# Performance work log

Measured on AMD Instinct MI355X. Metric: run time of the kernel, lower is better.

The kernel has to match this reference:

```python
import math
import jax, jax.numpy as jnp
import numpy as np

B, S, D, H = 2, 4096, 512, 8
DH = D // H


def setup_inputs() -> dict:
    key = jax.random.key(0)
    ks = jax.random.split(key, 12)
    lim = 1.0 / math.sqrt(D)
    u = lambda k, shp: jax.random.uniform(k, shp, jnp.float32, -lim, lim)
    return {
        "x": jax.random.normal(ks[0], (B, S, D), jnp.float32),
        "gamma": jax.random.uniform(ks[1], (B, S, 1), jnp.float32),
        "Wq": u(ks[2], (D, D)), "bq": u(ks[3], (D,)),
        "Wk": u(ks[4], (D, D)), "bk": u(ks[5], (D,)),
        "Wv": u(ks[6], (D, D)), "bv": u(ks[7], (D,)),
        "Wo": u(ks[8], (D, D)), "bo": u(ks[9], (D,)),
    }


def reference(x, gamma, Wq, bq, Wk, bk, Wv, bv, Wo, bo):
    b, s, d = x.shape
    # projections (torch Linear: x @ W.T + b), split heads -> [B,H,S,DH]
    def proj(W, bias):
        return (x @ W.T + bias).reshape(b, s, H, DH).transpose(0, 2, 1, 3)
    q, k, v = proj(Wq, bq), proj(Wk, bk), proj(Wv, bv)

    scores = jnp.einsum("bhsd,bhtd->bhst", q, k) / math.sqrt(DH)  # [B,H,S,S]
    causal = jnp.triu(jnp.ones((s, s), bool), k=1)  # True above diagonal
    neg_inf = jnp.float32(-jnp.inf)
    scores = jnp.where(causal[None, None], neg_inf, scores)

    # hyperbolic positional bias: -log1p(gamma_i * max(i-j, 0) + 1e-8)
    pos = jnp.arange(s)
    delta = jnp.clip(pos[:, None] - pos[None, :], 0).astype(jnp.float32)  # [S,S]
    gamma_q = gamma[:, :, 0][:, :, None]  # [B,S,1]
    hyper = -jnp.log1p(gamma_q * delta + 1e-8)  # [B,S,S]
    hyper = jnp.where(causal[None], neg_inf, hyper)
    scores = scores + hyper[:, None]  # [B,H,S,S]

    attn = jax.nn.softmax(scores, axis=-1)
    out = jnp.einsum("bhst,bhtd->bhsd", attn, v)  # [B,H,S,DH]
    out = out.transpose(0, 2, 1, 3).reshape(b, s, d)
    return out @ Wo.T + bo
```

## Files before the change

### kernel.cpp

```cpp
#include <hip/hip_runtime.h>
#include <hip/hip_bf16.h>

#define Bb 2
#define Ss 4096
#define Dd 512
#define Hh 8
#define DHh 64

typedef __attribute__((ext_vector_type(8))) short short8;
typedef __attribute__((ext_vector_type(4))) float floatx4;

static __device__ __forceinline__ ushort bfbits(float f) {
  union { __hip_bfloat16 h; ushort u; } cv;
  cv.h = __float2bfloat16(f);
  return cv.u;
}

__global__ void cvt_all(const float* __restrict__ x,
                        const float* __restrict__ w0, const float* __restrict__ w1,
                        const float* __restrict__ w2, const float* __restrict__ w3,
                        ushort* __restrict__ out) {
  const int XN4 = (Bb * Ss * Dd) / 4;
  const int WN4 = (Dd * Dd) / 4;
  int i = blockIdx.x * blockDim.x + threadIdx.x;
  if (i >= XN4 + 4 * WN4) return;
  const float* s; int li;
  if (i < XN4) { s = x; li = i; }
  else {
    int t = i - XN4; int j = t >> 16; li = t & (WN4 - 1);
    s = (j == 0) ? w0 : (j == 1) ? w1 : (j == 2) ? w2 : w3;
  }
  float4 f = ((const float4*)s)[li];
  ushort4 u;
  u.x = bfbits(f.x); u.y = bfbits(f.y); u.z = bfbits(f.z); u.w = bfbits(f.w);
  ((ushort4*)out)[i] = u;
}

static __device__ __forceinline__ int vperm(int s0) {
  int kb = (s0 >> 4) & 3, gq = (s0 >> 2) & 3;
  return (s0 & ~63) | ((kb >> 1) << 5) | (gq << 3) | ((kb & 1) << 2);
}

#define LD32(buf, k0)                                                          \
  af[buf][0] = *(const short8*)(ap + (k0));                                    \
  af[buf][1] = *(const short8*)(ap + 16 * 512 + (k0));                         \
  _Pragma("unroll")                                                            \
  for (int ns = 0; ns < 4; ++ns)                                               \
    bfr[buf][ns] = *(const short8*)(bp + (size_t)ns * 16 * 512 + (k0));

__global__ __launch_bounds__(256) void qkv_gemm(
    const ushort* __restrict__ xb,
    const ushort* __restrict__ Wq, const ushort* __restrict__ Wk, const ushort* __restrict__ Wv,
    const float* __restrict__ bq, const float* __restrict__ bk, const float* __restrict__ bv,
    ushort* __restrict__ qo, ushort* __restrict__ ko, ushort* __restrict__ vo)
{
  int mb = blockIdx.x / 24, nbt = blockIdx.x % 24;
  int which = nbt >> 3, nb = nbt & 7;
  const ushort* Bw  = (which == 0) ? Wq : (which == 1) ? Wk : Wv;
  const float* bias = (which == 0) ? bq : (which == 1) ? bk : bv;
  int lane = threadIdx.x & 63, w = threadIdx.x >> 6;
  int g = lane >> 4, ln = lane & 15;
  int m0 = mb * 128 + w * 32;
  const ushort* ap = xb + (size_t)(m0 + ln) * 512 + g * 8;
  const ushort* bp = Bw + (size_t)(nb * 64 + ln) * 512 + g * 8;
  floatx4 acc[2][4] = {};
  short8 af[2][2], bfr[2][4];
  LD32(0, 0)
#pragma unroll
  for (int it = 0; it < 16; ++it) {
    int cur = it & 1;
    if (it < 15) { LD32(cur ^ 1, (it + 1) * 32) }
#pragma unroll
    for (int ns = 0; ns < 4; ++ns) {
      acc[0][ns] = __builtin_amdgcn_mfma_f32_16x16x32_bf16(af[cur][0], bfr[cur][ns], acc[0][ns], 0, 0, 0);
      acc[1][ns] = __builtin_amdgcn_mfma_f32_16x16x32_bf16(af[cur][1], bfr[cur][ns], acc[1][ns], 0, 0, 0);
    }
  }
  float scale = (which == 0) ? 0.125f : 1.0f;
#pragma unroll
  for (int rb = 0; rb < 2; ++rb)
#pragma unroll
    for (int ns = 0; ns < 4; ++ns) {
      int col = nb * 64 + ns * 16 + ln;
      float bv_ = bias[col];
      int hh = col >> 6, dh = col & 63;
      if (which == 2) {
        int i0 = m0 + rb * 16 + g * 4;
        int bI = i0 >> 12, s0 = i0 & (Ss - 1);
        ushort4 pk;
        pk.x = bfbits(acc[rb][ns][0] + bv_);
        pk.y = bfbits(acc[rb][ns][1] + bv_);
        pk.z = bfbits(acc[rb][ns][2] + bv_);
        pk.w = bfbits(acc[rb][ns][3] + bv_);
        *(ushort4*)(vo + (((size_t)bI * Hh + hh) * DHh + dh) * Ss + vperm(s0)) = pk;
      } else {
        ushort* outp = (which == 0) ? qo : ko;
#pragma unroll
        for (int r = 0; r < 4; ++r) {
          int i = m0 + rb * 16 + g * 4 + r;
          int bI = i >> 12, s = i & (Ss - 1);
          outp[(((size_t)bI * Hh + hh) * Ss + s) * DHh + dh] = bfbits((acc[rb][ns][r] + bv_) * scale);
        }
      }
    }
}

__global__ __launch_bounds__(256) void gemm_out(
    const ushort* __restrict__ A, const ushort* __restrict__ Bw,
    const float* __restrict__ bias, float* __restrict__ outp)
{
  int mb = blockIdx.x >> 3, nb = blockIdx.x & 7;
  int lane = threadIdx.x & 63, w = threadIdx.x >> 6;
  int g = lane >> 4, ln = lane & 15;
  int m0 = mb * 128 + w * 32;
  const ushort* ap = A + (size_t)(m0 + ln) * 512 + g * 8;
  const ushort* bp = Bw + (size_t)(nb * 64 + ln) * 512 + g * 8;
  floatx4 acc[2][4] = {};
  short8 af[2][2], bfr[2][4];
  LD32(0, 0)
#pragma unroll
  for (int it = 0; it < 16; ++it) {
    int cur = it & 1;
    if (it < 15) { LD32(cur ^ 1, (it + 1) * 32) }
#pragma unroll
    for (int ns = 0; ns < 4; ++ns) {
      acc[0][ns] = __builtin_amdgcn_mfma_f32_16x16x32_bf16(af[cur][0], bfr[cur][ns], acc[0][ns], 0, 0, 0);
      acc[1][ns] = __builtin_amdgcn_mfma_f32_16x16x32_bf16(af[cur][1], bfr[cur][ns], acc[1][ns], 0, 0, 0);
    }
  }
#pragma unroll
  for (int rb = 0; rb < 2; ++rb)
#pragma unroll
    for (int ns = 0; ns < 4; ++ns) {
      int col = nb * 64 + ns * 16 + ln;
      float bv_ = bias[col];
#pragma unroll
      for (int r = 0; r < 4; ++r)
        outp[(size_t)(m0 + rb * 16 + g * 4 + r) * 512 + col] = acc[rb][ns][r] + bv_;
    }
}

__global__ __launch_bounds__(256, 2) void flash5(
    const ushort* __restrict__ q, const ushort* __restrict__ k,
    const ushort* __restrict__ vt, const float* __restrict__ gamma,
    ushort* __restrict__ o)
{
  __shared__ __align__(16) float Pmrg[2][64][34];
  __shared__ __align__(16) ushort Tb[2][16 * 72];

  int z = blockIdx.x;
  int j = (z ^ (z >> 8)) & 3;
  int bh = (z >> 2) & 15;
  int w16 = z >> 6;
  int u = (j == 0) ? w16 : (j == 1) ? 31 - w16 : (j == 2) ? 32 + w16 : 63 - w16;
  int b = bh >> 3, hh = bh & 7;
  int tid = threadIdx.x;
  int wv = tid >> 6, lane = tid & 63;
  int qsel = wv >> 1, half = wv & 1;
  int g = lane >> 4, ln = lane & 15;
  int t = 2 * u + qsel;
  int q0 = t * 32;
  int ktm = u;
  int nkt = u + 1;
  int h = (nkt + 1) >> 1;
  int lo = half ? h : 0, hi = half ? nkt : h;

  const ushort* qp = q + ((size_t)bh * Ss + q0 + ln) * DHh + g * 8;
  short8 qf00 = *(const short8*)qp;
  short8 qf01 = *(const short8*)(qp + 32);
  short8 qf10 = *(const short8*)(qp + 16 * DHh);
  short8 qf11 = *(const short8*)(qp + 16 * DHh + 32);

  const ushort* kp = k + ((size_t)bh * Ss + ln) * DHh + g * 8;
  const ushort* vp = vt + ((size_t)bh * DHh + ln) * Ss + g * 8;

  int qrow0 = q0 + ln, qrow1 = q0 + 16 + ln;
  float gm0 = gamma[(size_t)b * Ss + qrow0];
  float gm1 = gamma[(size_t)b * Ss + qrow1];
  float l2[2] = {0.0f, 0.0f};
  floatx4 oacc[2][4] = {};

  short8 kfl[4], kfh[4], vf[8];
  int kb0 = lo * 64;
#pragma unroll
  for (int ns = 0; ns < 4; ++ns) {
    kfl[ns] = *(const short8*)(kp + (size_t)(kb0 + ns * 16) * DHh);
    kfh[ns] = *(const short8*)(kp + (size_t)(kb0 + ns * 16) * DHh + 32);
  }
#pragma unroll
  for (int cc = 0; cc < 8; ++cc)
    vf[cc] = *(const short8*)(vp + (size_t)((cc & 3) * 16) * Ss + kb0 + (cc >> 2) * 32);

  for (int kt = lo; kt < hi; ++kt) {
    int kbase = kt * 64;
    float sv[2][16];
#pragma unroll
    for (int ns = 0; ns < 4; ++ns) {
      floatx4 z0 = {}, z1 = {};
      z0 = __builtin_amdgcn_mfma_f32_16x16x32_bf16(kfl[ns], qf00, z0, 0, 0, 0);
      z0 = __builtin_amdgcn_mfma_f32_16x16x32_bf16(kfh[ns], qf01, z0, 0, 0, 0);
      z1 = __builtin_amdgcn_mfma_f32_16x16x32_bf16(kfl[ns], qf10, z1, 0, 0, 0);
      z1 = __builtin_amdgcn_mfma_f32_16x16x32_bf16(kfh[ns], qf11, z1, 0, 0, 0);
#pragma unroll
      for (int r = 0; r < 4; ++r) { sv[0][ns * 4 + r] = z0[r]; sv[1][ns * 4 + r] = z1[r]; }
    }
    if (kt + 1 < hi) {
      const ushort* kn = kp + (size_t)(kbase + 64) * DHh;
#pragma unroll
      for (int ns = 0; ns < 4; ++ns) {
        kfl[ns] = *(const short8*)(kn + (size_t)(ns * 16) * DHh);
        kfh[ns] = *(const short8*)(kn + (size_t)(ns * 16) * DHh + 32);
      }
    }
    bool last = (kt == ktm);
    short8 pfrag[2][2];
#pragma unroll
    for (int qb = 0; qb < 2; ++qb) {
      int qrow = qb ? qrow1 : qrow0;
      float gm = qb ? gm1 : gm0;
      int db = qrow - kbase - g * 4;
      if (last) {
#pragma unroll
        for (int e = 0; e < 16; ++e)
          if (db - (e >> 2) * 16 - (e & 3) < 0) sv[qb][e] = -1e30f;
      }
      float rs = 0.0f;
#pragma unroll
      for (int e = 0; e < 16; ++e) {
        float delta = fmaxf((float)(db - (e >> 2) * 16 - (e & 3)), 0.0f);
        float wt = __builtin_amdgcn_rcpf(fmaf(gm, delta, 1.0f));
        float pv = __expf(sv[qb][e]) * wt;
        rs += pv;
        sv[qb][e] = pv;
      }
      l2[qb] += rs;
#pragma unroll
      for (int c = 0; c < 2; ++c) {
        short8 pk;
#pragma unroll
        for (int jj = 0; jj < 4; ++jj) {
          ((ushort*)&pk)[jj]     = bfbits(sv[qb][(2 * c) * 4 + jj]);
          ((ushort*)&pk)[jj + 4] = bfbits(sv[qb][(2 * c + 1) * 4 + jj]);
        }
        pfrag[qb][c] = pk;
      }
    }
#pragma unroll
    for (int c = 0; c < 2; ++c)
#pragma unroll
      for (int ds = 0; ds < 4; ++ds) {
        oacc[0][ds] = __builtin_amdgcn_mfma_f32_16x16x32_bf16(vf[c * 4 + ds], pfrag[0][c], oacc[0][ds], 0, 0, 0);
        oacc[1][ds] = __builtin_amdgcn_mfma_f32_16x16x32_bf16(vf[c * 4 + ds], pfrag[1][c], oacc[1][ds], 0, 0, 0);
      }
    if (kt + 1 < hi) {
#pragma unroll
      for (int cc = 0; cc < 8; ++cc)
        vf[cc] = *(const short8*)(vp + (size_t)((cc & 3) * 16) * Ss + kbase + 64 + (cc >> 2) * 32);
    }
  }

  if (half) {
#pragma unroll
    for (int qb = 0; qb < 2; ++qb)
#pragma unroll
      for (int ds = 0; ds < 4; ++ds)
#pragma unroll
        for (int r = 0; r < 4; ++r)
          Pmrg[qsel][lane][qb * 16 + ds * 4 + r] = oacc[qb][ds][r];
    Pmrg[qsel][lane][32] = l2[0];
    Pmrg[qsel][lane][33] = l2[1];
  }
  __syncthreads();
  if (!half) {
#pragma unroll
    for (int qb = 0; qb < 2; ++qb) {
#pragma unroll
      for (int ds = 0; ds < 4; ++ds)
#pragma unroll
        for (int r = 0; r < 4; ++r)
          oacc[qb][ds][r] += Pmrg[qsel][lane][qb * 16 + ds * 4 + r];
      float l = l2[qb] + Pmrg[qsel][lane][32 + qb];
      l += __shfl_xor(l, 16);
      l += __shfl_xor(l, 32);
      float linv = 1.0f / l;
      ushort* tb = &Tb[qsel][0];
#pragma unroll
      for (int ds = 0; ds < 4; ++ds)
#pragma unroll
        for (int r = 0; r < 4; ++r)
          tb[ln * 72 + ds * 16 + g * 4 + r] = bfbits(oacc[qb][ds][r] * linv);
      short8 v0 = *(const short8*)(tb + ln * 72 + g * 16);
      short8 v1 = *(const short8*)(tb + ln * 72 + g * 16 + 8);
      size_t oa = ((size_t)b * Ss + q0 + qb * 16 + ln) * Dd + hh * DHh + g * 16;
      *(short8*)(o + oa) = v0;
      *(short8*)(o + oa + 8) = v1;
    }
  }
}

extern "C" void kernel_launch(void* const* d_in, const int* in_sizes, int n_in,
                              void* d_out, int out_size, void* d_ws, size_t ws_size,
                              hipStream_t stream) {
  const float* x     = (const float*)d_in[0];
  const float* gamma = (const float*)d_in[1];
  const float* Wq    = (const float*)d_in[2];
  const float* bq    = (const float*)d_in[3];
  const float* Wk    = (const float*)d_in[4];
  const float* bk    = (const float*)d_in[5];
  const float* Wv    = (const float*)d_in[6];
  const float* bv    = (const float*)d_in[7];
  const float* Wo    = (const float*)d_in[8];
  const float* bo    = (const float*)d_in[9];

  const size_t NX = (size_t)Bb * Ss * Dd;
  const size_t NW = (size_t)Dd * Dd;
  ushort* xb  = (ushort*)d_ws;
  ushort* Wqb = xb + NX;
  ushort* Wkb = Wqb + NW;
  ushort* Wvb = Wkb + NW;
  ushort* Wob = Wvb + NW;
  ushort* qb  = Wob + NW;
  ushort* kb  = qb + NX;
  ushort* vtb = kb + NX;
  ushort* ab  = vtb + NX;

  const int total4 = (int)(NX / 4 + 4 * (NW / 4));
  cvt_all<<<(total4 + 255) / 256, 256, 0, stream>>>(x, Wq, Wk, Wv, Wo, xb);

  qkv_gemm<<<64 * 24, 256, 0, stream>>>(xb, Wqb, Wkb, Wvb, bq, bk, bv, qb, kb, vtb);

  flash5<<<1024, 256, 0, stream>>>(qb, kb, vtb, gamma, ab);

  gemm_out<<<512, 256, 0, stream>>>(ab, Wob, bo, (float*)d_out);
}
```

Before: 310.5 us.

## Enlarge QKV GEMM tiles, pair causal tiles per block, truncate bf16 packing

The QKV projection GEMM now gives each wave a 64x64 output tile (4x4 MFMA fragments), so each block covers 128x128 and half as many blocks launch, raising operand reuse per load. The flash attention kernel processes two complementary causal query tiles (u and 63-u) in one persistent block, which evens out work per block and halves the grid. It also changes how the key-tile split between the two halves is chosen in the second pass. P-fragment packing now truncates fp32 to bf16 by taking the high bits instead of rounding, which saves ALU work but adds a small precision bias.

```diff
diff --git a/kernel.cpp b/kernel.cpp
--- a/kernel.cpp
+++ b/kernel.cpp
@@ -14,6 +14,11 @@
   union { __hip_bfloat16 h; ushort u; } cv;
   cv.h = __float2bfloat16(f);
   return cv.u;
+}
+
+static __device__ __forceinline__ unsigned int packhi(float a, float b) {
+  union { float f; unsigned int u; } ca, cb; ca.f = a; cb.f = b;
+  return (ca.u >> 16) | (cb.u & 0xffff0000u);
 }
 
 __global__ void cvt_all(const float* __restrict__ x,
@@ -41,69 +46,79 @@
   return (s0 & ~63) | ((kb >> 1) << 5) | (gq << 3) | ((kb & 1) << 2);
 }
 
+#define LDQK(buf, k0)                                                          \
+  _Pragma("unroll")                                                            \
+  for (int rb = 0; rb < 4; ++rb)                                               \
+    af[buf][rb] = *(const short8*)(ap + (size_t)rb * 16 * 512 + (k0));         \
+  _Pragma("unroll")                                                            \
+  for (int cb = 0; cb < 4; ++cb)                                               \
+    bf[buf][cb] = *(const short8*)(bp + (size_t)cb * 16 * 512 + (k0));
+
+__global__ __launch_bounds__(256) void qkv_gemm(
+    const ushort* __restrict__ xb,
+    const ushort* __restrict__ Wq, const ushort* __restrict__ Wk, const ushort* __restrict__ Wv,
+    const float* __restrict__ bq, const float* __restrict__ bk, const float* __restrict__ bv,
+    ushort* __restrict__ qo, ushort* __restrict__ ko, ushort* __restrict__ vo)
+{
+  int mb = blockIdx.x / 12, rest = blockIdx.x % 12;
+  int which = rest >> 2, nb = rest & 3;
+  const ushort* Bw  = (which == 0) ? Wq : (which == 1) ? Wk : Wv;
+  const float* bias = (which == 0) ? bq : (which == 1) ? bk : bv;
+  int lane = threadIdx.x & 63, w = threadIdx.x >> 6;
+  int wr = w & 1, wc = w >> 1;
+  int g = lane >> 4, ln = lane & 15;
+  int m0 = mb * 128 + wr * 64;
+  int c0 = nb * 128 + wc * 64;
+  const ushort* ap = xb + (size_t)(m0 + ln) * 512 + g * 8;
+  const ushort* bp = Bw + (size_t)(c0 + ln) * 512 + g * 8;
+  floatx4 acc[4][4] = {};
+  short8 af[2][4], bf[2][4];
+  LDQK(0, 0)
+#pragma unroll
+  for (int it = 0; it < 16; ++it) {
+    int cur = it & 1;
+    if (it < 15) { LDQK(cur ^ 1, (it + 1) * 32) }
+#pragma unroll
+    for (int rb = 0; rb < 4; ++rb)
+#pragma unroll
+      for (int cb = 0; cb < 4; ++cb)
+        acc[rb][cb] = __builtin_amdgcn_mfma_f32_16x16x32_bf16(af[cur][rb], bf[cur][cb], acc[rb][cb], 0, 0, 0);
+  }
+  float scale = (which == 0) ? 0.125f : 1.0f;
+#pragma unroll
+  for (int rb = 0; rb < 4; ++rb)
+#pragma unroll
+    for (int cb = 0; cb < 4; ++cb) {
+      int col = c0 + cb * 16 + ln;
+      float bv_ = bias[col];
+      int hh = col >> 6, dh = col & 63;
+      if (which == 2) {
+        int i0 = m0 + rb * 16 + g * 4;
+        int bI = i0 >> 12, s0 = i0 & (Ss - 1);
+        ushort4 pk;
+        pk.x = bfbits(acc[rb][cb][0] + bv_);
+        pk.y = bfbits(acc[rb][cb][1] + bv_);
+        pk.z = bfbits(acc[rb][cb][2] + bv_);
+        pk.w = bfbits(acc[rb][cb][3] + bv_);
+        *(ushort4*)(vo + (((size_t)bI * Hh + hh) * DHh + dh) * Ss + vperm(s0)) = pk;
+      } else {
+        ushort* outp = (which == 0) ? qo : ko;
+#pragma unroll
+        for (int r = 0; r < 4; ++r) {
+          int i = m0 + rb * 16 + g * 4 + r;
+          int bI = i >> 12, s = i & (Ss - 1);
+          outp[(((size_t)bI * Hh + hh) * Ss + s) * DHh + dh] = bfbits((acc[rb][cb][r] + bv_) * scale);
+        }
+      }
+    }
+}
+
 #define LD32(buf, k0)                                                          \
   af[buf][0] = *(const short8*)(ap + (k0));                                    \
   af[buf][1] = *(const short8*)(ap + 16 * 512 + (k0));                         \
   _Pragma("unroll")                                                            \
   for (int ns = 0; ns < 4; ++ns)                                               \
     bfr[buf][ns] = *(const short8*)(bp + (size_t)ns * 16 * 512 + (k0));
-
-__global__ __launch_bounds__(256) void qkv_gemm(
-    const ushort* __restrict__ xb,
-    const ushort* __restrict__ Wq, const ushort* __restrict__ Wk, const ushort* __restrict__ Wv,
-    const float* __restrict__ bq, const float* __restrict__ bk, const float* __restrict__ bv,
-    ushort* __restrict__ qo, ushort* __restrict__ ko, ushort* __restrict__ vo)
-{
-  int mb = blockIdx.x / 24, nbt = blockIdx.x % 24;
-  int which = nbt >> 3, nb = nbt & 7;
-  const ushort* Bw  = (which == 0) ? Wq : (which == 1) ? Wk : Wv;
-  const float* bias = (which == 0) ? bq : (which == 1) ? bk : bv;
-  int lane = threadIdx.x & 63, w = threadIdx.x >> 6;
-  int g = lane >> 4, ln = lane & 15;
-  int m0 = mb * 128 + w * 32;
-  const ushort* ap = xb + (size_t)(m0 + ln) * 512 + g * 8;
-  const ushort* bp = Bw + (size_t)(nb * 64 + ln) * 512 + g * 8;
-  floatx4 acc[2][4] = {};
-  short8 af[2][2], bfr[2][4];
-  LD32(0, 0)
-#pragma unroll
-  for (int it = 0; it < 16; ++it) {
-    int cur = it & 1;
-    if (it < 15) { LD32(cur ^ 1, (it + 1) * 32) }
-#pragma unroll
-    for (int ns = 0; ns < 4; ++ns) {
-      acc[0][ns] = __builtin_amdgcn_mfma_f32_16x16x32_bf16(af[cur][0], bfr[cur][ns], acc[0][ns], 0, 0, 0);
-      acc[1][ns] = __builtin_amdgcn_mfma_f32_16x16x32_bf16(af[cur][1], bfr[cur][ns], acc[1][ns], 0, 0, 0);
-    }
-  }
-  float scale = (which == 0) ? 0.125f : 1.0f;
-#pragma unroll
-  for (int rb = 0; rb < 2; ++rb)
-#pragma unroll
-    for (int ns = 0; ns < 4; ++ns) {
-      int col = nb * 64 + ns * 16 + ln;
-      float bv_ = bias[col];
-      int hh = col >> 6, dh = col & 63;
-      if (which == 2) {
-        int i0 = m0 + rb * 16 + g * 4;
-        int bI = i0 >> 12, s0 = i0 & (Ss - 1);
-        ushort4 pk;
-        pk.x = bfbits(acc[rb][ns][0] + bv_);
-        pk.y = bfbits(acc[rb][ns][1] + bv_);
-        pk.z = bfbits(acc[rb][ns][2] + bv_);
-        pk.w = bfbits(acc[rb][ns][3] + bv_);
-        *(ushort4*)(vo + (((size_t)bI * Hh + hh) * DHh + dh) * Ss + vperm(s0)) = pk;
-      } else {
-        ushort* outp = (which == 0) ? qo : ko;
-#pragma unroll
-        for (int r = 0; r < 4; ++r) {
-          int i = m0 + rb * 16 + g * 4 + r;
-          int bI = i >> 12, s = i & (Ss - 1);
-          outp[(((size_t)bI * Hh + hh) * Ss + s) * DHh + dh] = bfbits((acc[rb][ns][r] + bv_) * scale);
-        }
-      }
-    }
-}
 
 __global__ __launch_bounds__(256) void gemm_out(
     const ushort* __restrict__ A, const ushort* __restrict__ Bw,
@@ -140,7 +155,7 @@
     }
 }
 
-__global__ __launch_bounds__(256, 2) void flash5(
+__global__ __launch_bounds__(256, 2) void flash6(
     const ushort* __restrict__ q, const ushort* __restrict__ k,
     const ushort* __restrict__ vt, const float* __restrict__ gamma,
     ushort* __restrict__ o)
@@ -149,151 +164,154 @@
   __shared__ __align__(16) ushort Tb[2][16 * 72];
 
   int z = blockIdx.x;
-  int j = (z ^ (z >> 8)) & 3;
-  int bh = (z >> 2) & 15;
-  int w16 = z >> 6;
-  int u = (j == 0) ? w16 : (j == 1) ? 31 - w16 : (j == 2) ? 32 + w16 : 63 - w16;
+  int bh = z & 15, up = z >> 4;
   int b = bh >> 3, hh = bh & 7;
   int tid = threadIdx.x;
   int wv = tid >> 6, lane = tid & 63;
   int qsel = wv >> 1, half = wv & 1;
   int g = lane >> 4, ln = lane & 15;
-  int t = 2 * u + qsel;
-  int q0 = t * 32;
-  int ktm = u;
-  int nkt = u + 1;
-  int h = (nkt + 1) >> 1;
-  int lo = half ? h : 0, hi = half ? nkt : h;
-
-  const ushort* qp = q + ((size_t)bh * Ss + q0 + ln) * DHh + g * 8;
-  short8 qf00 = *(const short8*)qp;
-  short8 qf01 = *(const short8*)(qp + 32);
-  short8 qf10 = *(const short8*)(qp + 16 * DHh);
-  short8 qf11 = *(const short8*)(qp + 16 * DHh + 32);
 
   const ushort* kp = k + ((size_t)bh * Ss + ln) * DHh + g * 8;
   const ushort* vp = vt + ((size_t)bh * DHh + ln) * Ss + g * 8;
 
-  int qrow0 = q0 + ln, qrow1 = q0 + 16 + ln;
-  float gm0 = gamma[(size_t)b * Ss + qrow0];
-  float gm1 = gamma[(size_t)b * Ss + qrow1];
-  float l2[2] = {0.0f, 0.0f};
-  floatx4 oacc[2][4] = {};
-
-  short8 kfl[4], kfh[4], vf[8];
-  int kb0 = lo * 64;
-#pragma unroll
-  for (int ns = 0; ns < 4; ++ns) {
-    kfl[ns] = *(const short8*)(kp + (size_t)(kb0 + ns * 16) * DHh);
-    kfh[ns] = *(const short8*)(kp + (size_t)(kb0 + ns * 16) * DHh + 32);
-  }
-#pragma unroll
-  for (int cc = 0; cc < 8; ++cc)
-    vf[cc] = *(const short8*)(vp + (size_t)((cc & 3) * 16) * Ss + kb0 + (cc >> 2) * 32);
-
-  for (int kt = lo; kt < hi; ++kt) {
-    int kbase = kt * 64;
-    float sv[2][16];
+#pragma unroll 1
+  for (int rep = 0; rep < 2; ++rep) {
+    int u = rep ? (63 - up) : up;
+    int t = 2 * u + qsel;
+    int q0 = t * 32;
+    int ktm = u;
+    int nkt = u + 1;
+    int h = (nkt + 1 - rep) >> 1;
+    int lo = half ? h : 0, hi = half ? nkt : h;
+
+    const ushort* qp = q + ((size_t)bh * Ss + q0 + ln) * DHh + g * 8;
+    short8 qf00 = *(const short8*)qp;
+    short8 qf01 = *(const short8*)(qp + 32);
+    short8 qf10 = *(const short8*)(qp + 16 * DHh);
+    short8 qf11 = *(const short8*)(qp + 16 * DHh + 32);
+
+    int qrow0 = q0 + ln, qrow1 = q0 + 16 + ln;
+    float gm0 = gamma[(size_t)b * Ss + qrow0];
+    float gm1 = gamma[(size_t)b * Ss + qrow1];
+    float l2[2] = {0.0f, 0.0f};
+    floatx4 oacc[2][4] = {};
+
+    short8 kfl[4], kfh[4], vf[8];
+    int kb0 = lo * 64;
 #pragma unroll
     for (int ns = 0; ns < 4; ++ns) {
-      floatx4 z0 = {}, z1 = {};
-      z0 = __builtin_amdgcn_mfma_f32_16x16x32_bf16(kfl[ns], qf00, z0, 0, 0, 0);
-      z0 = __builtin_amdgcn_mfma_f32_16x16x32_bf16(kfh[ns], qf01, z0, 0, 0, 0);
-      z1 = __builtin_amdgcn_mfma_f32_16x16x32_bf16(kfl[ns], qf10, z1, 0, 0, 0);
-      z1 = __builtin_amdgcn_mfma_f32_16x16x32_bf16(kfh[ns], qf11, z1, 0, 0, 0);
-#pragma unroll
-      for (int r = 0; r < 4; ++r) { sv[0][ns * 4 + r] = z0[r]; sv[1][ns * 4 + r] = z1[r]; }
-    }
-    if (kt + 1 < hi) {
-      const ushort* kn = kp + (size_t)(kbase + 64) * DHh;
+      kfl[ns] = *(const short8*)(kp + (size_t)(kb0 + ns * 16) * DHh);
+      kfh[ns] = *(const short8*)(kp + (size_t)(kb0 + ns * 16) * DHh + 32);
+    }
+#pragma unroll
+    for (int cc = 0; cc < 8; ++cc)
+      vf[cc] = *(const short8*)(vp + (size_t)((cc & 3) * 16) * Ss + kb0 + (cc >> 2) * 32);
+
+    for (int kt = lo; kt < hi; ++kt) {
+      int kbase = kt * 64;
+      float sv[2][16];
 #pragma unroll
       for (int ns = 0; ns < 4; ++ns) {
-        kfl[ns] = *(const short8*)(kn + (size_t)(ns * 16) * DHh);
-        kfh[ns] = *(const short8*)(kn + (size_t)(ns * 16) * DHh + 32);
-      }
-    }
-    bool last = (kt == ktm);
-    short8 pfrag[2][2];
-#pragma unroll
-    for (int qb = 0; qb < 2; ++qb) {
-      int qrow = qb ? qrow1 : qrow0;
-      float gm = qb ? gm1 : gm0;
-      int db = qrow - kbase - g * 4;
-      if (last) {
-#pragma unroll
-        for (int e = 0; e < 16; ++e)
-          if (db - (e >> 2) * 16 - (e & 3) < 0) sv[qb][e] = -1e30f;
-      }
-      float rs = 0.0f;
-#pragma unroll
-      for (int e = 0; e < 16; ++e) {
-        float delta = fmaxf((float)(db - (e >> 2) * 16 - (e & 3)), 0.0f);
-        float wt = __builtin_amdgcn_rcpf(fmaf(gm, delta, 1.0f));
-        float pv = __expf(sv[qb][e]) * wt;
-        rs += pv;
-        sv[qb][e] = pv;
-      }
-      l2[qb] += rs;
-#pragma unroll
-      for (int c = 0; c < 2; ++c) {
-        short8 pk;
-#pragma unroll
-        for (int jj = 0; jj < 4; ++jj) {
-          ((ushort*)&pk)[jj]     = bfbits(sv[qb][(2 * c) * 4 + jj]);
-          ((ushort*)&pk)[jj + 4] = bfbits(sv[qb][(2 * c + 1) * 4 + jj]);
-        }
-        pfrag[qb][c] = pk;
-      }
-    }
-#pragma unroll
-    for (int c = 0; c < 2; ++c)
-#pragma unroll
-      for (int ds = 0; ds < 4; ++ds) {
-        oacc[0][ds] = __builtin_amdgcn_mfma_f32_16x16x32_bf16(vf[c * 4 + ds], pfrag[0][c], oacc[0][ds], 0, 0, 0);
-        oacc[1][ds] = __builtin_amdgcn_mfma_f32_16x16x32_bf16(vf[c * 4 + ds], pfrag[1][c], oacc[1][ds], 0, 0, 0);
-      }
-    if (kt + 1 < hi) {
-#pragma unroll
-      for (int cc = 0; cc < 8; ++cc)
-        vf[cc] = *(const short8*)(vp + (size_t)((cc & 3) * 16) * Ss + kbase + 64 + (cc >> 2) * 32);
-    }
-  }
-
-  if (half) {
-#pragma unroll
-    for (int qb = 0; qb < 2; ++qb)
-#pragma unroll
-      for (int ds = 0; ds < 4; ++ds)
-#pragma unroll
-        for (int r = 0; r < 4; ++r)
-          Pmrg[qsel][lane][qb * 16 + ds * 4 + r] = oacc[qb][ds][r];
-    Pmrg[qsel][lane][32] = l2[0];
-    Pmrg[qsel][lane][33] = l2[1];
-  }
-  __syncthreads();
-  if (!half) {
-#pragma unroll
-    for (int qb = 0; qb < 2; ++qb) {
-#pragma unroll
-      for (int ds = 0; ds < 4; ++ds)
-#pragma unroll
-        for (int r = 0; r < 4; ++r)
-          oacc[qb][ds][r] += Pmrg[qsel][lane][qb * 16 + ds * 4 + r];
-      float l = l2[qb] + Pmrg[qsel][lane][32 + qb];
-      l += __shfl_xor(l, 16);
-      l += __shfl_xor(l, 32);
-      float linv = 1.0f / l;
-      ushort* tb = &Tb[qsel][0];
-#pragma unroll
-      for (int ds = 0; ds < 4; ++ds)
-#pragma unroll
-        for (int r = 0; r < 4; ++r)
-          tb[ln * 72 + ds * 16 + g * 4 + r] = bfbits(oacc[qb][ds][r] * linv);
-      short8 v0 = *(const short8*)(tb + ln * 72 + g * 16);
-      short8 v1 = *(const short8*)(tb + ln * 72 + g * 16 + 8);
-      size_t oa = ((size_t)b * Ss + q0 + qb * 16 + ln) * Dd + hh * DHh + g * 16;
-      *(short8*)(o + oa) = v0;
-      *(short8*)(o + oa + 8) = v1;
+        floatx4 z0 = {}, z1 = {};
+        z0 = __builtin_amdgcn_mfma_f32_16x16x32_bf16(kfl[ns], qf00, z0, 0, 0, 0);
+        z0 = __builtin_amdgcn_mfma_f32_16x16x32_bf16(kfh[ns], qf01, z0, 0, 0, 0);
+        z1 = __builtin_amdgcn_mfma_f32_16x16x32_bf16(kfl[ns], qf10, z1, 0, 0, 0);
+        z1 = __builtin_amdgcn_mfma_f32_16x16x32_bf16(kfh[ns], qf11, z1, 0, 0, 0);
+#pragma unroll
+        for (int r = 0; r < 4; ++r) { sv[0][ns * 4 + r] = z0[r]; sv[1][ns * 4 + r] = z1[r]; }
+      }
+      if (kt + 1 < hi) {
+        const ushort* kn = kp + (size_t)(kbase + 64) * DHh;
+#pragma unroll
+        for (int ns = 0; ns < 4; ++ns) {
+          kfl[ns] = *(const short8*)(kn + (size_t)(ns * 16) * DHh);
+          kfh[ns] = *(const short8*)(kn + (size_t)(ns * 16) * DHh + 32);
+        }
+      }
+      bool last = (kt == ktm);
+      short8 pfrag[2][2];
+#pragma unroll
+      for (int qb = 0; qb < 2; ++qb) {
+        int qrow = qb ? qrow1 : qrow0;
+        float gm = qb ? gm1 : gm0;
+        int db = qrow - kbase - g * 4;
+        if (last) {
+#pragma unroll
+          for (int e = 0; e < 16; ++e)
+            if (db - (e >> 2) * 16 - (e & 3) < 0) sv[qb][e] = -1e30f;
+        }
+        float fd = (float)db;
+        float rs = 0.0f;
+#pragma unroll
+        for (int e = 0; e < 16; ++e) {
+          float delta = fmaxf(fd - (float)((e >> 2) * 16 + (e & 3)), 0.0f);
+          float wt = __builtin_amdgcn_rcpf(fmaf(gm, delta, 1.0f));
+          float pv = __expf(sv[qb][e]) * wt;
+          rs += pv;
+          sv[qb][e] = pv;
+        }
+        l2[qb] += rs;
+#pragma unroll
+        for (int c = 0; c < 2; ++c) {
+          uint4 pkd;
+          pkd.x = packhi(sv[qb][8 * c + 0], sv[qb][8 * c + 1]);
+          pkd.y = packhi(sv[qb][8 * c + 2], sv[qb][8 * c + 3]);
+          pkd.z = packhi(sv[qb][8 * c + 4], sv[qb][8 * c + 5]);
+          pkd.w = packhi(sv[qb][8 * c + 6], sv[qb][8 * c + 7]);
+          pfrag[qb][c] = *(short8*)&pkd;
+        }
+      }
+#pragma unroll
+      for (int c = 0; c < 2; ++c)
+#pragma unroll
+        for (int ds = 0; ds < 4; ++ds) {
+          oacc[0][ds] = __builtin_amdgcn_mfma_f32_16x16x32_bf16(vf[c * 4 + ds], pfrag[0][c], oacc[0][ds], 0, 0, 0);
+          oacc[1][ds] = __builtin_amdgcn_mfma_f32_16x16x32_bf16(vf[c * 4 + ds], pfrag[1][c], oacc[1][ds], 0, 0, 0);
+        }
+      if (kt + 1 < hi) {
+#pragma unroll
+        for (int cc = 0; cc < 8; ++cc)
+          vf[cc] = *(const short8*)(vp + (size_t)((cc & 3) * 16) * Ss + kbase + 64 + (cc >> 2) * 32);
+      }
+    }
+
+    __syncthreads();
+    if (half) {
+#pragma unroll
+      for (int qb = 0; qb < 2; ++qb)
+#pragma unroll
+        for (int ds = 0; ds < 4; ++ds)
+#pragma unroll
+          for (int r = 0; r < 4; ++r)
+            Pmrg[qsel][lane][qb * 16 + ds * 4 + r] = oacc[qb][ds][r];
+      Pmrg[qsel][lane][32] = l2[0];
+      Pmrg[qsel][lane][33] = l2[1];
+    }
+    __syncthreads();
+    if (!half) {
+#pragma unroll
+      for (int qb = 0; qb < 2; ++qb) {
+#pragma unroll
+        for (int ds = 0; ds < 4; ++ds)
+#pragma unroll
+          for (int r = 0; r < 4; ++r)
+            oacc[qb][ds][r] += Pmrg[qsel][lane][qb * 16 + ds * 4 + r];
+        float l = l2[qb] + Pmrg[qsel][lane][32 + qb];
+        l += __shfl_xor(l, 16);
+        l += __shfl_xor(l, 32);
+        float linv = 1.0f / l;
+        ushort* tb = &Tb[qsel][0];
+#pragma unroll
+        for (int ds = 0; ds < 4; ++ds)
+#pragma unroll
+          for (int r = 0; r < 4; ++r)
+            tb[ln * 72 + ds * 16 + g * 4 + r] = bfbits(oacc[qb][ds][r] * linv);
+        short8 v0 = *(const short8*)(tb + ln * 72 + g * 16);
+        short8 v1 = *(const short8*)(tb + ln * 72 + g * 16 + 8);
+        size_t oa = ((size_t)b * Ss + q0 + qb * 16 + ln) * Dd + hh * DHh + g * 16;
+        *(short8*)(o + oa) = v0;
+        *(short8*)(o + oa + 8) = v1;
+      }
     }
   }
 }
@@ -327,9 +345,9 @@
   const int total4 = (int)(NX / 4 + 4 * (NW / 4));
   cvt_all<<<(total4 + 255) / 256, 256, 0, stream>>>(x, Wq, Wk, Wv, Wo, xb);
 
-  qkv_gemm<<<64 * 24, 256, 0, stream>>>(xb, Wqb, Wkb, Wvb, bq, bk, bv, qb, kb, vtb);
-
-  flash5<<<1024, 256, 0, stream>>>(qb, kb, vtb, gamma, ab);
+  qkv_gemm<<<64 * 12, 256, 0, stream>>>(xb, Wqb, Wkb, Wvb, bq, bk, bv, qb, kb, vtb);
+
+  flash6<<<512, 256, 0, stream>>>(qb, kb, vtb, gamma, ab);
 
   gemm_out<<<512, 256, 0, stream>>>(ab, Wob, bo, (float*)d_out);
 }
```

Measured after the change: 282.7 us. -9.0%, faster.
